# Kernel optimization log

Measured on AMD Instinct MI355X. Metric: run time of the kernel, lower is better.

Reference implementation:

```python
import jax, jax.numpy as jnp
import numpy as np

N_NODES = 50000
N_EDGES = 1600000
HID = 256
NODE_F = 2
EDGE_F = 7
NUM_LAYERS = 3
EPS = 0.0  # GINEConv default eps


def _glorot(key, shape):
    fan_in, fan_out = shape[0], shape[1]
    lim = float(np.sqrt(6.0 / (fan_in + fan_out)))
    return jax.random.uniform(key, shape, jnp.float32, -lim, lim)


def setup_inputs() -> dict:
    key = jax.random.key(0)
    ks = jax.random.split(key, 16)
    x = jax.random.normal(ks[0], (N_NODES, NODE_F), jnp.float32)
    edge_index = jax.random.randint(ks[1], (2, N_EDGES), 0, N_NODES, jnp.int64)
    edge_attr = jax.random.normal(ks[2], (N_EDGES, EDGE_F), jnp.float32)
    # conv1: lin_edge1 (7->2), nn1 Linear(2->HID)
    We1 = _glorot(ks[3], (EDGE_F, NODE_F)); be1 = jnp.zeros((NODE_F,), jnp.float32)
    W1 = _glorot(ks[4], (NODE_F, HID));     b1 = jnp.zeros((HID,), jnp.float32)
    # conv2: lin_edge2 (7->HID), nn2 Linear(HID->HID)
    We2 = _glorot(ks[5], (EDGE_F, HID));    be2 = jnp.zeros((HID,), jnp.float32)
    W2 = _glorot(ks[6], (HID, HID));        b2 = jnp.zeros((HID,), jnp.float32)
    # endLinear HID->1
    Wend = _glorot(ks[7], (HID, 1));        bend = jnp.zeros((1,), jnp.float32)
    return dict(x=x, edge_index=edge_index, edge_attr=edge_attr,
                We1=We1, be1=be1, W1=W1, b1=b1,
                We2=We2, be2=be2, W2=W2, b2=b2,
                Wend=Wend, bend=bend)


def _gine_conv(h, src, dst, edge_emb, W, b):
    # message: relu(h[src] + lin_edge(edge_attr)); aggregate: scatter-sum at dst
    msg = jax.nn.relu(h[src] + edge_emb)                      # [E, C]
    aggr = jax.ops.segment_sum(msg, dst, num_segments=N_NODES)  # [N, C]
    return ((1.0 + EPS) * h + aggr) @ W + b                   # nn(...)


def reference(x, edge_index, edge_attr, We1, be1, W1, b1, We2, be2, W2, b2, Wend, bend):
    src, dst = edge_index[0], edge_index[1]
    # layer 1
    h = _gine_conv(x, src, dst, edge_attr @ We1 + be1, W1, b1)
    # layers 2..num_layers (shared conv2 weights, batchnorm disabled)
    edge_emb2 = edge_attr @ We2 + be2
    for _ in range(NUM_LAYERS - 1):
        h = jax.nn.relu(h)
        h = _gine_conv(h, src, dst, edge_emb2, W2, b2)
    h = jax.nn.relu(h)
    return jax.nn.sigmoid(h @ Wend + bend)  # [N, 1]
```

## Files before the change

kernel.cpp:

```cpp
#include <hip/hip_runtime.h>
#include <hip/hip_fp16.h>
#include <math.h>

#define N_NODES 50000
#define N_EDGES 1600000
#define HID 256
#define SCAN_B 196

typedef _Float16 f16x8 __attribute__((ext_vector_type(8)));
typedef float f32x4 __attribute__((ext_vector_type(4)));
typedef float v2f __attribute__((ext_vector_type(2)));

static __device__ __forceinline__ __half2 pk_max2(__half2 a, __half2 b) {
    unsigned au = *reinterpret_cast<unsigned*>(&a);
    unsigned bu = *reinterpret_cast<unsigned*>(&b);
    unsigned r;
    asm("v_pk_max_f16 %0, %1, %2" : "=v"(r) : "v"(au), "v"(bu));
    return *reinterpret_cast<__half2*>(&r);
}

static __device__ __forceinline__ unsigned pack4_fp8(float a, float b, float c, float d) {
    int v = __builtin_amdgcn_cvt_pk_fp8_f32(a, b, 0, false);
    v = __builtin_amdgcn_cvt_pk_fp8_f32(c, d, v, true);
    return (unsigned)v;
}

__global__ __launch_bounds__(256) void hist_kernel(const int* __restrict__ dst,
                                                   int* __restrict__ deg) {
    const int T = gridDim.x * 256;
    const int t = blockIdx.x * 256 + threadIdx.x;
#pragma unroll
    for (int i = 0; i < 4; ++i) {
        int e = t + i * T;
        if (e < N_EDGES) atomicAdd(&deg[dst[e]], 1);
    }
}

__global__ __launch_bounds__(256) void scan1_kernel(const int* __restrict__ deg,
                                                    int* __restrict__ bsum) {
    int idx = blockIdx.x * 256 + threadIdx.x;
    int v = (idx < N_NODES) ? deg[idx] : 0;
#pragma unroll
    for (int off = 32; off > 0; off >>= 1) v += __shfl_down(v, off);
    __shared__ int ws[4];
    if ((threadIdx.x & 63) == 0) ws[threadIdx.x >> 6] = v;
    __syncthreads();
    if (threadIdx.x == 0) bsum[blockIdx.x] = ws[0] + ws[1] + ws[2] + ws[3];
}

__global__ __launch_bounds__(256) void scan2_kernel(int* __restrict__ bsum) {
    __shared__ int s[256];
    int t = threadIdx.x;
    int v = (t < SCAN_B) ? bsum[t] : 0;
    s[t] = v;
    __syncthreads();
    for (int off = 1; off < 256; off <<= 1) {
        int u = (t >= off) ? s[t - off] : 0;
        __syncthreads();
        s[t] += u;
        __syncthreads();
    }
    if (t < SCAN_B) bsum[t] = s[t] - v;
}

__global__ __launch_bounds__(256) void scan3_kernel(const int* __restrict__ deg,
                                                    const int* __restrict__ bsum,
                                                    int* __restrict__ base) {
    __shared__ int s[256];
    int t = threadIdx.x;
    int idx = blockIdx.x * 256 + t;
    int v = (idx < N_NODES) ? deg[idx] : 0;
    s[t] = v;
    __syncthreads();
    for (int off = 1; off < 256; off <<= 1) {
        int u = (t >= off) ? s[t - off] : 0;
        __syncthreads();
        s[t] += u;
        __syncthreads();
    }
    if (idx < N_NODES) base[idx] = bsum[blockIdx.x] + s[t] - v;
    if (idx == 0) base[N_NODES] = N_EDGES;
}

static __device__ __forceinline__ void write_rec(float* __restrict__ rec, int pos,
                                                 const float* __restrict__ ep, int s) {
    float4 v0, v1;
    *(__half2*)&v0.x = __floats2half2_rn(ep[0], ep[0]);
    *(__half2*)&v0.y = __floats2half2_rn(ep[1], ep[1]);
    *(__half2*)&v0.z = __floats2half2_rn(ep[2], ep[2]);
    *(__half2*)&v0.w = __floats2half2_rn(ep[3], ep[3]);
    *(__half2*)&v1.x = __floats2half2_rn(ep[4], ep[4]);
    *(__half2*)&v1.y = __floats2half2_rn(ep[5], ep[5]);
    *(__half2*)&v1.z = __floats2half2_rn(ep[6], ep[6]);
    v1.w = __int_as_float(s);
    float* rp = rec + (size_t)pos * 8;
    *(float4*)rp       = v0;
    *(float4*)(rp + 4) = v1;
}

__global__ __launch_bounds__(256) void scatter_rec_kernel(
        const int* __restrict__ src,
        const int* __restrict__ dst,
        const float* __restrict__ ea,
        const int* __restrict__ base,
        int* __restrict__ cursor,
        float* __restrict__ rec) {
    const int T = gridDim.x * 256;
    const int t = blockIdx.x * 256 + threadIdx.x;
    const int e0 = t, e1 = t + T, e2 = t + 2 * T, e3 = t + 3 * T;
    const bool v3 = (e3 < N_EDGES);
    int d0 = dst[e0], d1 = dst[e1], d2 = dst[e2];
    int s0 = src[e0], s1 = src[e1], s2 = src[e2];
    int d3 = v3 ? dst[e3] : 0;
    int s3 = v3 ? src[e3] : 0;
    int p0 = base[d0] + atomicAdd(&cursor[d0], 1);
    int p1 = base[d1] + atomicAdd(&cursor[d1], 1);
    int p2 = base[d2] + atomicAdd(&cursor[d2], 1);
    int p3 = v3 ? (base[d3] + atomicAdd(&cursor[d3], 1)) : 0;
    write_rec(rec, p0, ea + (size_t)e0 * 7, s0);
    write_rec(rec, p1, ea + (size_t)e1 * 7, s1);
    write_rec(rec, p2, ea + (size_t)e2 * 7, s2);
    if (v3) write_rec(rec, p3, ea + (size_t)e3 * 7, s3);
}

__global__ __launch_bounds__(256) void layer1_kernel(
        const float* __restrict__ x,
        const float* __restrict__ rec,
        const int* __restrict__ base,
        const float* __restrict__ We1,
        const float* __restrict__ be1,
        const float* __restrict__ W1,
        const float* __restrict__ b1,
        unsigned* __restrict__ h8) {
    const int lane = threadIdx.x & 63;
    const int wid = threadIdx.x >> 6;
    const int n = blockIdx.x * 4 + wid;
    if (n >= N_NODES) return;
    float w00 = We1[0],  w01 = We1[1],  w10 = We1[2],  w11 = We1[3];
    float w20 = We1[4],  w21 = We1[5],  w30 = We1[6],  w31 = We1[7];
    float w40 = We1[8],  w41 = We1[9],  w50 = We1[10], w51 = We1[11];
    float w60 = We1[12], w61 = We1[13];
    float bb0 = be1[0], bb1 = be1[1];
    float m0 = 0.f, m1 = 0.f;
    const int s0 = base[n], s1 = base[n + 1];
    for (int pos = s0 + lane; pos < s1; pos += 64) {
        const float* p = rec + (size_t)pos * 8;
        float4 a = *(const float4*)p;
        float4 b = *(const float4*)(p + 4);
        int s = __float_as_int(b.w);
        float a0 = __low2float(*(__half2*)&a.x);
        float a1 = __low2float(*(__half2*)&a.y);
        float a2 = __low2float(*(__half2*)&a.z);
        float a3 = __low2float(*(__half2*)&a.w);
        float a4 = __low2float(*(__half2*)&b.x);
        float a5 = __low2float(*(__half2*)&b.y);
        float a6 = __low2float(*(__half2*)&b.z);
        float t0 = bb0, t1 = bb1;
        t0 = fmaf(a0, w00, t0); t1 = fmaf(a0, w01, t1);
        t0 = fmaf(a1, w10, t0); t1 = fmaf(a1, w11, t1);
        t0 = fmaf(a2, w20, t0); t1 = fmaf(a2, w21, t1);
        t0 = fmaf(a3, w30, t0); t1 = fmaf(a3, w31, t1);
        t0 = fmaf(a4, w40, t0); t1 = fmaf(a4, w41, t1);
        t0 = fmaf(a5, w50, t0); t1 = fmaf(a5, w51, t1);
        t0 = fmaf(a6, w60, t0); t1 = fmaf(a6, w61, t1);
        float2 xv = *(const float2*)&x[(size_t)s * 2];
        m0 += fmaxf(t0 + xv.x, 0.f);
        m1 += fmaxf(t1 + xv.y, 0.f);
    }
#pragma unroll
    for (int off = 32; off > 0; off >>= 1) {
        m0 += __shfl_down(m0, off);
        m1 += __shfl_down(m1, off);
    }
    m0 = __shfl(m0, 0);
    m1 = __shfl(m1, 0);
    const float t0 = x[n * 2 + 0] + m0;
    const float t1 = x[n * 2 + 1] + m1;
    const int c = lane * 4;
    float4 wa = *(const float4*)&W1[c];
    float4 wb = *(const float4*)&W1[256 + c];
    float4 bv = *(const float4*)&b1[c];
    float4 r;
    r.x = fmaxf(fmaf(t0, wa.x, fmaf(t1, wb.x, bv.x)), 0.f);
    r.y = fmaxf(fmaf(t0, wa.y, fmaf(t1, wb.y, bv.y)), 0.f);
    r.z = fmaxf(fmaf(t0, wa.z, fmaf(t1, wb.z, bv.z)), 0.f);
    r.w = fmaxf(fmaf(t0, wa.w, fmaf(t1, wb.w, bv.w)), 0.f);
    h8[(size_t)n * 64 + lane] = pack4_fp8(r.x, r.y, r.z, r.w);
}

#define EDGEH(RA, RB, HU)                                              \
    do {                                                               \
        __half2 _a0 = *(__half2*)&RA.x, _a1 = *(__half2*)&RA.y;        \
        __half2 _a2 = *(__half2*)&RA.z, _a3 = *(__half2*)&RA.w;        \
        __half2 _a4 = *(__half2*)&RB.x, _a5 = *(__half2*)&RB.y;        \
        __half2 _a6 = *(__half2*)&RB.z;                                \
        __half2 _m0 = bb01, _m1 = bb23;                                \
        _m0 = __hfma2(_a0, w0a, _m0); _m1 = __hfma2(_a0, w0b, _m1);    \
        _m0 = __hfma2(_a1, w1a, _m0); _m1 = __hfma2(_a1, w1b, _m1);    \
        _m0 = __hfma2(_a2, w2a, _m0); _m1 = __hfma2(_a2, w2b, _m1);    \
        _m0 = __hfma2(_a3, w3a, _m0); _m1 = __hfma2(_a3, w3b, _m1);    \
        _m0 = __hfma2(_a4, w4a, _m0); _m1 = __hfma2(_a4, w4b, _m1);    \
        _m0 = __hfma2(_a5, w5a, _m0); _m1 = __hfma2(_a5, w5b, _m1);    \
        _m0 = __hfma2(_a6, w6a, _m0); _m1 = __hfma2(_a6, w6b, _m1);    \
        v2f _hf0 = __builtin_amdgcn_cvt_pk_f32_fp8((int)(HU), false);  \
        v2f _hf1 = __builtin_amdgcn_cvt_pk_f32_fp8((int)(HU), true);   \
        __half2 _h0 = __float22half2_rn(make_float2(_hf0.x, _hf0.y));  \
        __half2 _h1 = __float22half2_rn(make_float2(_hf1.x, _hf1.y));  \
        _m0 = pk_max2(__hadd2(_m0, _h0), z2);                          \
        _m1 = pk_max2(__hadd2(_m1, _h1), z2);                          \
        acc0 = __hadd2(acc0, _m0);                                     \
        acc1 = __hadd2(acc1, _m1);                                     \
    } while (0)

#define HLOAD(RB) (h8[(size_t)__builtin_amdgcn_readfirstlane(          \
                       __float_as_int(RB.w)) * 64 + lane])

#define LOADG(A0, B0, A1, B1, A2, B2, A3, B3, H0, H1, H2, H3, G)       \
    do {                                                               \
        const float4* _rp = rp + (size_t)(G) * 8;                      \
        A0 = _rp[0]; B0 = _rp[1]; A1 = _rp[2]; B1 = _rp[3];            \
        A2 = _rp[4]; B2 = _rp[5]; A3 = _rp[6]; B3 = _rp[7];            \
        H0 = HLOAD(B0); H1 = HLOAD(B1);                                \
        H2 = HLOAD(B2); H3 = HLOAD(B3);                                \
    } while (0)

#define CONS4(A0, B0, A1, B1, A2, B2, A3, B3, H0, H1, H2, H3)          \
    do {                                                               \
        EDGEH(A0, B0, H0); EDGEH(A1, B1, H1);                          \
        EDGEH(A2, B2, H2); EDGEH(A3, B3, H3);                          \
    } while (0)

__global__ __launch_bounds__(256) void aggr2_kernel(
        const unsigned* __restrict__ h8,
        const float* __restrict__ rec,
        const int* __restrict__ base,
        const float* __restrict__ We2,
        const float* __restrict__ be2,
        __half* __restrict__ accum) {
    const int lane = threadIdx.x & 63;
    const int n = blockIdx.x * 4 + (threadIdx.x >> 6);
    if (n >= N_NODES) return;
    const int c4 = lane * 4;
    __half2 w0a = __floats2half2_rn(We2[0 * HID + c4], We2[0 * HID + c4 + 1]);
    __half2 w0b = __floats2half2_rn(We2[0 * HID + c4 + 2], We2[0 * HID + c4 + 3]);
    __half2 w1a = __floats2half2_rn(We2[1 * HID + c4], We2[1 * HID + c4 + 1]);
    __half2 w1b = __floats2half2_rn(We2[1 * HID + c4 + 2], We2[1 * HID + c4 + 3]);
    __half2 w2a = __floats2half2_rn(We2[2 * HID + c4], We2[2 * HID + c4 + 1]);
    __half2 w2b = __floats2half2_rn(We2[2 * HID + c4 + 2], We2[2 * HID + c4 + 3]);
    __half2 w3a = __floats2half2_rn(We2[3 * HID + c4], We2[3 * HID + c4 + 1]);
    __half2 w3b = __floats2half2_rn(We2[3 * HID + c4 + 2], We2[3 * HID + c4 + 3]);
    __half2 w4a = __floats2half2_rn(We2[4 * HID + c4], We2[4 * HID + c4 + 1]);
    __half2 w4b = __floats2half2_rn(We2[4 * HID + c4 + 2], We2[4 * HID + c4 + 3]);
    __half2 w5a = __floats2half2_rn(We2[5 * HID + c4], We2[5 * HID + c4 + 1]);
    __half2 w5b = __floats2half2_rn(We2[5 * HID + c4 + 2], We2[5 * HID + c4 + 3]);
    __half2 w6a = __floats2half2_rn(We2[6 * HID + c4], We2[6 * HID + c4 + 1]);
    __half2 w6b = __floats2half2_rn(We2[6 * HID + c4 + 2], We2[6 * HID + c4 + 3]);
    __half2 bb01 = __floats2half2_rn(be2[c4], be2[c4 + 1]);
    __half2 bb23 = __floats2half2_rn(be2[c4 + 2], be2[c4 + 3]);
    const __half2 z2 = __float2half2_rn(0.f);

    __half2 acc0, acc1;
    {
        unsigned hv = h8[(size_t)n * 64 + lane];
        v2f f0 = __builtin_amdgcn_cvt_pk_f32_fp8((int)hv, false);
        v2f f1 = __builtin_amdgcn_cvt_pk_f32_fp8((int)hv, true);
        acc0 = __float22half2_rn(make_float2(f0.x, f0.y));
        acc1 = __float22half2_rn(make_float2(f1.x, f1.y));
    }
    const int s0 = __builtin_amdgcn_readfirstlane(base[n]);
    const int deg = __builtin_amdgcn_readfirstlane(base[n + 1]) - s0;
    const float4* rp = (const float4*)rec + (size_t)s0 * 2;
    const int ng = deg >> 2;

    float4 r0a, r0b, r1a, r1b, r2a, r2b, r3a, r3b;
    unsigned rh0, rh1, rh2, rh3;
    float4 t0a, t0b, t1a, t1b, t2a, t2b, t3a, t3b;
    unsigned th0, th1, th2, th3;

    if (ng > 0) {
        LOADG(r0a, r0b, r1a, r1b, r2a, r2b, r3a, r3b, rh0, rh1, rh2, rh3, 0);
        int g = 1;
        for (; g + 1 < ng; g += 2) {
            LOADG(t0a, t0b, t1a, t1b, t2a, t2b, t3a, t3b, th0, th1, th2, th3, g);
            CONS4(r0a, r0b, r1a, r1b, r2a, r2b, r3a, r3b, rh0, rh1, rh2, rh3);
            LOADG(r0a, r0b, r1a, r1b, r2a, r2b, r3a, r3b, rh0, rh1, rh2, rh3, g + 1);
            CONS4(t0a, t0b, t1a, t1b, t2a, t2b, t3a, t3b, th0, th1, th2, th3);
        }
        if (g < ng) {
            LOADG(t0a, t0b, t1a, t1b, t2a, t2b, t3a, t3b, th0, th1, th2, th3, g);
            CONS4(r0a, r0b, r1a, r1b, r2a, r2b, r3a, r3b, rh0, rh1, rh2, rh3);
            CONS4(t0a, t0b, t1a, t1b, t2a, t2b, t3a, t3b, th0, th1, th2, th3);
        } else {
            CONS4(r0a, r0b, r1a, r1b, r2a, r2b, r3a, r3b, rh0, rh1, rh2, rh3);
        }
    }
    for (int i = ng * 4; i < deg; ++i) {
        float4 ra = rp[(size_t)i * 2], rbv = rp[(size_t)i * 2 + 1];
        unsigned hv = HLOAD(rbv);
        EDGEH(ra, rbv, hv);
    }
    float2 of;
    *(__half2*)&of.x = acc0;
    *(__half2*)&of.y = acc1;
    *(float2*)&accum[(size_t)n * HID + c4] = of;
}

__global__ __launch_bounds__(256) void w2_swizzle_kernel(const float* __restrict__ W,
                                                         __half* __restrict__ W2s) {
    int t = blockIdx.x * 256 + threadIdx.x;
    if (t >= 16 * 8 * 64) return;
    int lane = t & 63;
    int kc = (t >> 6) & 7;
    int ct = t >> 9;
    int k0 = kc * 32 + (lane >> 4) * 8;
    int col = ct * 16 + (lane & 15);
#pragma unroll
    for (int j = 0; j < 8; ++j)
        W2s[(size_t)t * 8 + j] = __float2half(W[(size_t)(k0 + j) * HID + col]);
}

template <bool FUSE_END>
__global__ __launch_bounds__(256) void node2_mfma_kernel(
        const __half* __restrict__ A,
        const __half* __restrict__ W2s,
        const float* __restrict__ b,
        unsigned char* __restrict__ h8,
        const float* __restrict__ Wend,
        const float* __restrict__ bend,
        float* __restrict__ out) {
    const int lane = threadIdx.x & 63;
    const int wv = threadIdx.x >> 6;
    const int n_base = blockIdx.x * 64 + wv * 16;
    if (n_base >= N_NODES) return;
    const int quad = lane >> 4;
    const int mrow = lane & 15;
    f16x8 af[8];
    const __half* ap = A + (size_t)(n_base + mrow) * HID + quad * 8;
#pragma unroll
    for (int kc = 0; kc < 8; ++kc)
        af[kc] = *(const f16x8*)(ap + kc * 32);
    float p0 = 0.f, p1 = 0.f, p2 = 0.f, p3 = 0.f;
#pragma unroll
    for (int ct = 0; ct < 16; ++ct) {
        f32x4 c = {0.f, 0.f, 0.f, 0.f};
        const f16x8* bp = (const f16x8*)W2s + (size_t)(ct * 8) * 64 + lane;
#pragma unroll
        for (int kc = 0; kc < 8; ++kc)
            c = __builtin_amdgcn_mfma_f32_16x16x32_f16(af[kc], bp[(size_t)kc * 64],
                                                       c, 0, 0, 0);
        const int col = ct * 16 + mrow;
        const float bias = b[col];
        if (!FUSE_END) {
#pragma unroll
            for (int r = 0; r < 4; ++r) {
                int n = n_base + quad * 4 + r;
                float v = fmaxf(c[r] + bias, 0.f);
                int pk = __builtin_amdgcn_cvt_pk_fp8_f32(v, v, 0, false);
                if (n < N_NODES)
                    h8[(size_t)n * HID + col] = (unsigned char)(pk & 0xff);
            }
        } else {
            const float we = Wend[col];
            p0 = fmaf(fmaxf(c[0] + bias, 0.f), we, p0);
            p1 = fmaf(fmaxf(c[1] + bias, 0.f), we, p1);
            p2 = fmaf(fmaxf(c[2] + bias, 0.f), we, p2);
            p3 = fmaf(fmaxf(c[3] + bias, 0.f), we, p3);
        }
    }
    if (FUSE_END) {
#pragma unroll
        for (int mask = 1; mask < 16; mask <<= 1) {
            p0 += __shfl_xor(p0, mask);
            p1 += __shfl_xor(p1, mask);
            p2 += __shfl_xor(p2, mask);
            p3 += __shfl_xor(p3, mask);
        }
        if (mrow == 0) {
            const float bd = bend[0];
            int n = n_base + quad * 4;
            if (n + 0 < N_NODES) out[n + 0] = 1.f / (1.f + expf(-(p0 + bd)));
            if (n + 1 < N_NODES) out[n + 1] = 1.f / (1.f + expf(-(p1 + bd)));
            if (n + 2 < N_NODES) out[n + 2] = 1.f / (1.f + expf(-(p2 + bd)));
            if (n + 3 < N_NODES) out[n + 3] = 1.f / (1.f + expf(-(p3 + bd)));
        }
    }
}

extern "C" void kernel_launch(void* const* d_in, const int* in_sizes, int n_in,
                              void* d_out, int out_size, void* d_ws, size_t ws_size,
                              hipStream_t stream) {
    const float* x    = (const float*)d_in[0];
    const int*   ei   = (const int*)d_in[1];
    const float* ea   = (const float*)d_in[2];
    const float* We1  = (const float*)d_in[3];
    const float* be1  = (const float*)d_in[4];
    const float* W1   = (const float*)d_in[5];
    const float* b1   = (const float*)d_in[6];
    const float* We2  = (const float*)d_in[7];
    const float* be2  = (const float*)d_in[8];
    const float* W2   = (const float*)d_in[9];
    const float* b2   = (const float*)d_in[10];
    const float* Wend = (const float*)d_in[11];
    const float* bend = (const float*)d_in[12];
    float* out = (float*)d_out;

    const int* src = ei;
    const int* dst = ei + N_EDGES;

    const size_t HN = (size_t)N_NODES * HID;
    __half*   Bh   = (__half*)d_ws;
    unsigned* Ah   = (unsigned*)(Bh + HN);
    float*    rec  = (float*)(Ah + (size_t)N_NODES * 64);
    __half*   W2s  = (__half*)(rec + (size_t)N_EDGES * 8);
    int*   deg    = (int*)(W2s + 16 * 8 * 64 * 8);
    int*   cursor = deg + N_NODES;
    int*   base   = cursor + N_NODES;
    int*   bsum   = base + N_NODES + 2;

    const int E4_B = (N_EDGES + 4 * 256 - 1) / (4 * 256);

    hipMemsetAsync(deg, 0, (size_t)N_NODES * 2 * sizeof(int), stream);
    hist_kernel<<<E4_B, 256, 0, stream>>>(dst, deg);
    scan1_kernel<<<SCAN_B, 256, 0, stream>>>(deg, bsum);
    scan2_kernel<<<1, 256, 0, stream>>>(bsum);
    scan3_kernel<<<SCAN_B, 256, 0, stream>>>(deg, bsum, base);
    scatter_rec_kernel<<<E4_B, 256, 0, stream>>>(src, dst, ea, base, cursor, rec);
    w2_swizzle_kernel<<<32, 256, 0, stream>>>(W2, W2s);

    layer1_kernel<<<(N_NODES + 3) / 4, 256, 0, stream>>>(x, rec, base, We1, be1,
                                                         W1, b1, Ah);

    const int N2_B = (N_NODES + 63) / 64;
    aggr2_kernel<<<(N_NODES + 3) / 4, 256, 0, stream>>>(Ah, rec, base, We2, be2, Bh);
    node2_mfma_kernel<false><<<N2_B, 256, 0, stream>>>(Bh, W2s, b2,
                                                       (unsigned char*)Ah,
                                                       nullptr, nullptr, nullptr);
    aggr2_kernel<<<(N_NODES + 3) / 4, 256, 0, stream>>>(Ah, rec, base, We2, be2, Bh);
    node2_mfma_kernel<true><<<N2_B, 256, 0, stream>>>(Bh, W2s, b2, nullptr,
                                                      Wend, bend, out);
}
```

Measured before the change: 541.9 us.

## Pack edge records into 16 bytes with a 16-bit source index

Each per-edge CSR record shrinks from two float4s to one. The seven edge features are stored as packed half pairs, and the source node id goes in the upper 16 bits of the last word. The aggregation kernels unpack the halves with byte-permute splats, and layer 1 reads lo/hi halves directly. Separately, the scan kernel initialises the cursor to the base offsets, so the scatter kernel no longer has to load base. This cuts record write and read traffic and shortens the memset, but it relies on the node count fitting in 16 bits.

New measurement: 568.6 us. +4.9%, slower.

```diff
diff --git a/kernel.cpp b/kernel.cpp
--- a/kernel.cpp
+++ b/kernel.cpp
@@ -16,6 +16,15 @@
     unsigned bu = *reinterpret_cast<unsigned*>(&b);
     unsigned r;
     asm("v_pk_max_f16 %0, %1, %2" : "=v"(r) : "v"(au), "v"(bu));
+    return *reinterpret_cast<__half2*>(&r);
+}
+
+static __device__ __forceinline__ __half2 splat_lo(unsigned u) {
+    unsigned r = __builtin_amdgcn_perm(u, u, 0x01000100u);
+    return *reinterpret_cast<__half2*>(&r);
+}
+static __device__ __forceinline__ __half2 splat_hi(unsigned u) {
+    unsigned r = __builtin_amdgcn_perm(u, u, 0x03020302u);
     return *reinterpret_cast<__half2*>(&r);
 }
 
@@ -65,7 +74,8 @@
 
 __global__ __launch_bounds__(256) void scan3_kernel(const int* __restrict__ deg,
                                                     const int* __restrict__ bsum,
-                                                    int* __restrict__ base) {
+                                                    int* __restrict__ base,
+                                                    int* __restrict__ cursor) {
     __shared__ int s[256];
     int t = threadIdx.x;
     int idx = blockIdx.x * 256 + t;
@@ -78,31 +88,30 @@
         s[t] += u;
         __syncthreads();
     }
-    if (idx < N_NODES) base[idx] = bsum[blockIdx.x] + s[t] - v;
+    if (idx < N_NODES) {
+        int bv = bsum[blockIdx.x] + s[t] - v;
+        base[idx] = bv;
+        cursor[idx] = bv;
+    }
     if (idx == 0) base[N_NODES] = N_EDGES;
 }
 
 static __device__ __forceinline__ void write_rec(float* __restrict__ rec, int pos,
                                                  const float* __restrict__ ep, int s) {
-    float4 v0, v1;
-    *(__half2*)&v0.x = __floats2half2_rn(ep[0], ep[0]);
-    *(__half2*)&v0.y = __floats2half2_rn(ep[1], ep[1]);
-    *(__half2*)&v0.z = __floats2half2_rn(ep[2], ep[2]);
-    *(__half2*)&v0.w = __floats2half2_rn(ep[3], ep[3]);
-    *(__half2*)&v1.x = __floats2half2_rn(ep[4], ep[4]);
-    *(__half2*)&v1.y = __floats2half2_rn(ep[5], ep[5]);
-    *(__half2*)&v1.z = __floats2half2_rn(ep[6], ep[6]);
-    v1.w = __int_as_float(s);
-    float* rp = rec + (size_t)pos * 8;
-    *(float4*)rp       = v0;
-    *(float4*)(rp + 4) = v1;
+    float4 v;
+    *(__half2*)&v.x = __floats2half2_rn(ep[0], ep[1]);
+    *(__half2*)&v.y = __floats2half2_rn(ep[2], ep[3]);
+    *(__half2*)&v.z = __floats2half2_rn(ep[4], ep[5]);
+    unsigned w = (unsigned)__half_as_ushort(__float2half_rn(ep[6])) |
+                 ((unsigned)s << 16);
+    v.w = __uint_as_float(w);
+    *(float4*)(rec + (size_t)pos * 4) = v;
 }
 
 __global__ __launch_bounds__(256) void scatter_rec_kernel(
         const int* __restrict__ src,
         const int* __restrict__ dst,
         const float* __restrict__ ea,
-        const int* __restrict__ base,
         int* __restrict__ cursor,
         float* __restrict__ rec) {
     const int T = gridDim.x * 256;
@@ -113,10 +122,10 @@
     int s0 = src[e0], s1 = src[e1], s2 = src[e2];
     int d3 = v3 ? dst[e3] : 0;
     int s3 = v3 ? src[e3] : 0;
-    int p0 = base[d0] + atomicAdd(&cursor[d0], 1);
-    int p1 = base[d1] + atomicAdd(&cursor[d1], 1);
-    int p2 = base[d2] + atomicAdd(&cursor[d2], 1);
-    int p3 = v3 ? (base[d3] + atomicAdd(&cursor[d3], 1)) : 0;
+    int p0 = atomicAdd(&cursor[d0], 1);
+    int p1 = atomicAdd(&cursor[d1], 1);
+    int p2 = atomicAdd(&cursor[d2], 1);
+    int p3 = v3 ? atomicAdd(&cursor[d3], 1) : 0;
     write_rec(rec, p0, ea + (size_t)e0 * 7, s0);
     write_rec(rec, p1, ea + (size_t)e1 * 7, s1);
     write_rec(rec, p2, ea + (size_t)e2 * 7, s2);
@@ -144,17 +153,17 @@
     float m0 = 0.f, m1 = 0.f;
     const int s0 = base[n], s1 = base[n + 1];
     for (int pos = s0 + lane; pos < s1; pos += 64) {
-        const float* p = rec + (size_t)pos * 8;
-        float4 a = *(const float4*)p;
-        float4 b = *(const float4*)(p + 4);
-        int s = __float_as_int(b.w);
-        float a0 = __low2float(*(__half2*)&a.x);
-        float a1 = __low2float(*(__half2*)&a.y);
-        float a2 = __low2float(*(__half2*)&a.z);
-        float a3 = __low2float(*(__half2*)&a.w);
-        float a4 = __low2float(*(__half2*)&b.x);
-        float a5 = __low2float(*(__half2*)&b.y);
-        float a6 = __low2float(*(__half2*)&b.z);
+        float4 a = *(const float4*)(rec + (size_t)pos * 4);
+        __half2 hx = *(__half2*)&a.x;
+        __half2 hy = *(__half2*)&a.y;
+        __half2 hz = *(__half2*)&a.z;
+        __half2 hw = *(__half2*)&a.w;
+        unsigned uw = __float_as_uint(a.w);
+        int s = (int)(uw >> 16);
+        float a0 = __low2float(hx),  a1 = __high2float(hx);
+        float a2 = __low2float(hy),  a3 = __high2float(hy);
+        float a4 = __low2float(hz),  a5 = __high2float(hz);
+        float a6 = __low2float(hw);
         float t0 = bb0, t1 = bb1;
         t0 = fmaf(a0, w00, t0); t1 = fmaf(a0, w01, t1);
         t0 = fmaf(a1, w10, t0); t1 = fmaf(a1, w11, t1);
@@ -188,12 +197,16 @@
     h8[(size_t)n * 64 + lane] = pack4_fp8(r.x, r.y, r.z, r.w);
 }
 
-#define EDGEH(RA, RB, HU)                                              \
+#define EDGEH(RA, HU)                                                  \
     do {                                                               \
-        __half2 _a0 = *(__half2*)&RA.x, _a1 = *(__half2*)&RA.y;        \
-        __half2 _a2 = *(__half2*)&RA.z, _a3 = *(__half2*)&RA.w;        \
-        __half2 _a4 = *(__half2*)&RB.x, _a5 = *(__half2*)&RB.y;        \
-        __half2 _a6 = *(__half2*)&RB.z;                                \
+        unsigned _ux = __float_as_uint(RA.x);                          \
+        unsigned _uy = __float_as_uint(RA.y);                          \
+        unsigned _uz = __float_as_uint(RA.z);                          \
+        unsigned _uw = __float_as_uint(RA.w);                          \
+        __half2 _a0 = splat_lo(_ux), _a1 = splat_hi(_ux);              \
+        __half2 _a2 = splat_lo(_uy), _a3 = splat_hi(_uy);              \
+        __half2 _a4 = splat_lo(_uz), _a5 = splat_hi(_uz);              \
+        __half2 _a6 = splat_lo(_uw);                                   \
         __half2 _m0 = bb01, _m1 = bb23;                                \
         _m0 = __hfma2(_a0, w0a, _m0); _m1 = __hfma2(_a0, w0b, _m1);    \
         _m0 = __hfma2(_a1, w1a, _m0); _m1 = __hfma2(_a1, w1b, _m1);    \
@@ -212,22 +225,21 @@
         acc1 = __hadd2(acc1, _m1);                                     \
     } while (0)
 
-#define HLOAD(RB) (h8[(size_t)__builtin_amdgcn_readfirstlane(          \
-                       __float_as_int(RB.w)) * 64 + lane])
-
-#define LOADG(A0, B0, A1, B1, A2, B2, A3, B3, H0, H1, H2, H3, G)       \
+#define HLOAD(RA) (h8[(size_t)((unsigned)__builtin_amdgcn_readfirstlane(       \
+                       __float_as_int(RA.w)) >> 16) * 64 + lane])
+
+#define LOADG(A0, A1, A2, A3, H0, H1, H2, H3, G)                       \
     do {                                                               \
-        const float4* _rp = rp + (size_t)(G) * 8;                      \
-        A0 = _rp[0]; B0 = _rp[1]; A1 = _rp[2]; B1 = _rp[3];            \
-        A2 = _rp[4]; B2 = _rp[5]; A3 = _rp[6]; B3 = _rp[7];            \
-        H0 = HLOAD(B0); H1 = HLOAD(B1);                                \
-        H2 = HLOAD(B2); H3 = HLOAD(B3);                                \
+        const float4* _p = rp + (size_t)(G) * 4;                       \
+        A0 = _p[0]; A1 = _p[1]; A2 = _p[2]; A3 = _p[3];                \
+        H0 = HLOAD(A0); H1 = HLOAD(A1);                                \
+        H2 = HLOAD(A2); H3 = HLOAD(A3);                                \
     } while (0)
 
-#define CONS4(A0, B0, A1, B1, A2, B2, A3, B3, H0, H1, H2, H3)          \
+#define CONS4(A0, A1, A2, A3, H0, H1, H2, H3)                          \
     do {                                                               \
-        EDGEH(A0, B0, H0); EDGEH(A1, B1, H1);                          \
-        EDGEH(A2, B2, H2); EDGEH(A3, B3, H3);                          \
+        EDGEH(A0, H0); EDGEH(A1, H1);                                  \
+        EDGEH(A2, H2); EDGEH(A3, H3);                                  \
     } while (0)
 
 __global__ __launch_bounds__(256) void aggr2_kernel(
@@ -269,35 +281,35 @@
     }
     const int s0 = __builtin_amdgcn_readfirstlane(base[n]);
     const int deg = __builtin_amdgcn_readfirstlane(base[n + 1]) - s0;
-    const float4* rp = (const float4*)rec + (size_t)s0 * 2;
+    const float4* rp = (const float4*)rec + (size_t)s0;
     const int ng = deg >> 2;
 
-    float4 r0a, r0b, r1a, r1b, r2a, r2b, r3a, r3b;
+    float4 r0, r1, r2, r3;
     unsigned rh0, rh1, rh2, rh3;
-    float4 t0a, t0b, t1a, t1b, t2a, t2b, t3a, t3b;
+    float4 t0, t1, t2, t3;
     unsigned th0, th1, th2, th3;
 
     if (ng > 0) {
-        LOADG(r0a, r0b, r1a, r1b, r2a, r2b, r3a, r3b, rh0, rh1, rh2, rh3, 0);
+        LOADG(r0, r1, r2, r3, rh0, rh1, rh2, rh3, 0);
         int g = 1;
         for (; g + 1 < ng; g += 2) {
-            LOADG(t0a, t0b, t1a, t1b, t2a, t2b, t3a, t3b, th0, th1, th2, th3, g);
-            CONS4(r0a, r0b, r1a, r1b, r2a, r2b, r3a, r3b, rh0, rh1, rh2, rh3);
-            LOADG(r0a, r0b, r1a, r1b, r2a, r2b, r3a, r3b, rh0, rh1, rh2, rh3, g + 1);
-            CONS4(t0a, t0b, t1a, t1b, t2a, t2b, t3a, t3b, th0, th1, th2, th3);
+            LOADG(t0, t1, t2, t3, th0, th1, th2, th3, g);
+            CONS4(r0, r1, r2, r3, rh0, rh1, rh2, rh3);
+            LOADG(r0, r1, r2, r3, rh0, rh1, rh2, rh3, g + 1);
+            CONS4(t0, t1, t2, t3, th0, th1, th2, th3);
         }
         if (g < ng) {
-            LOADG(t0a, t0b, t1a, t1b, t2a, t2b, t3a, t3b, th0, th1, th2, th3, g);
-            CONS4(r0a, r0b, r1a, r1b, r2a, r2b, r3a, r3b, rh0, rh1, rh2, rh3);
-            CONS4(t0a, t0b, t1a, t1b, t2a, t2b, t3a, t3b, th0, th1, th2, th3);
+            LOADG(t0, t1, t2, t3, th0, th1, th2, th3, g);
+            CONS4(r0, r1, r2, r3, rh0, rh1, rh2, rh3);
+            CONS4(t0, t1, t2, t3, th0, th1, th2, th3);
         } else {
-            CONS4(r0a, r0b, r1a, r1b, r2a, r2b, r3a, r3b, rh0, rh1, rh2, rh3);
+            CONS4(r0, r1, r2, r3, rh0, rh1, rh2, rh3);
         }
     }
     for (int i = ng * 4; i < deg; ++i) {
-        float4 ra = rp[(size_t)i * 2], rbv = rp[(size_t)i * 2 + 1];
-        unsigned hv = HLOAD(rbv);
-        EDGEH(ra, rbv, hv);
+        float4 ra = rp[(size_t)i];
+        unsigned hv = HLOAD(ra);
+        EDGEH(ra, hv);
     }
     float2 of;
     *(__half2*)&of.x = acc0;
@@ -411,7 +423,7 @@
     __half*   Bh   = (__half*)d_ws;
     unsigned* Ah   = (unsigned*)(Bh + HN);
     float*    rec  = (float*)(Ah + (size_t)N_NODES * 64);
-    __half*   W2s  = (__half*)(rec + (size_t)N_EDGES * 8);
+    __half*   W2s  = (__half*)(rec + (size_t)N_EDGES * 4);
     int*   deg    = (int*)(W2s + 16 * 8 * 64 * 8);
     int*   cursor = deg + N_NODES;
     int*   base   = cursor + N_NODES;
@@ -419,12 +431,12 @@
 
     const int E4_B = (N_EDGES + 4 * 256 - 1) / (4 * 256);
 
-    hipMemsetAsync(deg, 0, (size_t)N_NODES * 2 * sizeof(int), stream);
+    hipMemsetAsync(deg, 0, (size_t)N_NODES * sizeof(int), stream);
     hist_kernel<<<E4_B, 256, 0, stream>>>(dst, deg);
     scan1_kernel<<<SCAN_B, 256, 0, stream>>>(deg, bsum);
     scan2_kernel<<<1, 256, 0, stream>>>(bsum);
-    scan3_kernel<<<SCAN_B, 256, 0, stream>>>(deg, bsum, base);
-    scatter_rec_kernel<<<E4_B, 256, 0, stream>>>(src, dst, ea, base, cursor, rec);
+    scan3_kernel<<<SCAN_B, 256, 0, stream>>>(deg, bsum, base, cursor);
+    scatter_rec_kernel<<<E4_B, 256, 0, stream>>>(src, dst, ea, cursor, rec);
     w2_swizzle_kernel<<<32, 256, 0, stream>>>(W2, W2s);
 
     layer1_kernel<<<(N_NODES + 3) / 4, 256, 0, stream>>>(x, rec, base, We1, be1,
```
